# Optimization experiments

Measured on AMD Instinct MI355X. Metric: run time of the kernel, lower is better.

Reference implementation:

```python
import jax, jax.numpy as jnp
import numpy as np

FEATURE_DIM = 256
KEEP = 64  # low-frequency block size kept after the pseudo-DCT


def setup_inputs() -> dict:
    key = jax.random.key(0)
    k_x, k_w, k_b = jax.random.split(key, 3)
    B, C, H, W = 32, 3, 512, 512
    x = jax.random.uniform(k_x, (B, C, H, W), dtype=jnp.float32)
    # nn.Linear(64*64, feature_dim): weight [out, in], bias [out]
    fan_in = KEEP * KEEP
    bound = 1.0 / np.sqrt(fan_in)
    fc_w = jax.random.uniform(k_w, (FEATURE_DIM, fan_in), dtype=jnp.float32, minval=-bound, maxval=bound)
    fc_b = jax.random.uniform(k_b, (FEATURE_DIM,), dtype=jnp.float32, minval=-bound, maxval=bound)
    return {"x": x, "fc_w": fc_w, "fc_b": fc_b}


def reference(x, fc_w, fc_b):
    # grayscale conversion (input has 3 channels)
    x_gray = 0.299 * x[:, 0] + 0.587 * x[:, 1] + 0.114 * x[:, 2]  # [B, H, W]
    # "dct2d": FFT along last dim, then FFT along second-to-last, real part
    X = jnp.fft.fft(jnp.fft.fft(x_gray, axis=-1), axis=-2).real  # [B, H, W]
    # keep low-frequency 64x64 block and flatten
    coeffs = X[:, :KEEP, :KEEP].reshape(x.shape[0], KEEP * KEEP)  # [B, 4096]
    # final linear projection
    return coeffs @ fc_w.T + fc_b  # [B, feature_dim]
```

## Files before the change

kernel.cpp:

```cpp
#include <hip/hip_runtime.h>

#define HW_ (512 * 512)
#define TWOPI_512 0.01227184630308513f

typedef __attribute__((ext_vector_type(8))) _Float16 half8;
typedef __attribute__((ext_vector_type(4))) _Float16 half4;
typedef __attribute__((ext_vector_type(4))) float    f32x4;

template<bool SIN>
__device__ __forceinline__ void k1_loop(const _Float16 (*g)[520],
                                        int l15, int quad, int mk0, int mk1,
                                        f32x4& acc0, f32x4& acc1)
{
    for (int k0 = 0; k0 < 512; k0 += 32) {
        int kc = k0 + quad * 8;
        half8 bv = *(const half8*)&g[l15][kc];
        half8 a0, a1;
#pragma unroll
        for (int j = 0; j < 8; ++j) {
            int k = kc + j;
            float ang0 = (float)(__mul24(mk0, k) & 511) * TWOPI_512;
            float ang1 = (float)(__mul24(mk1, k) & 511) * TWOPI_512;
            a0[j] = (_Float16)(SIN ? __sinf(ang0) : __cosf(ang0));
            a1[j] = (_Float16)(SIN ? __sinf(ang1) : __cosf(ang1));
        }
        acc0 = __builtin_amdgcn_mfma_f32_16x16x32_f16(a0, bv, acc0, 0, 0, 0);
        acc1 = __builtin_amdgcn_mfma_f32_16x16x32_f16(a1, bv, acc1, 0, 0, 0);
    }
}

__global__ __launch_bounds__(256) void k1(const float* __restrict__ x,
                                          const float* __restrict__ fc_w,
                                          _Float16* __restrict__ PF,
                                          _Float16* __restrict__ whF)
{
    __shared__ _Float16 g[16][520];
    int t = threadIdx.x;

    if (blockIdx.x == 32) {
        int pid = blockIdx.y;
        for (int it = 0; it < 16; ++it) {
            int idx8 = pid * 4096 + it * 256 + t;
            int lane = idx8 & 63;
            int f = ((idx8 >> 6) & 15) * 16 + (lane & 15);
            int k = (idx8 >> 10) * 32 + ((lane >> 4) << 3);
            const float* wp = fc_w + (size_t)f * 4096 + k;
            float4 f0 = *(const float4*)wp;
            float4 f1 = *(const float4*)(wp + 4);
            half8 o;
            o[0] = (_Float16)(f0.x * 16.0f);
            o[1] = (_Float16)(f0.y * 16.0f);
            o[2] = (_Float16)(f0.z * 16.0f);
            o[3] = (_Float16)(f0.w * 16.0f);
            o[4] = (_Float16)(f1.x * 16.0f);
            o[5] = (_Float16)(f1.y * 16.0f);
            o[6] = (_Float16)(f1.z * 16.0f);
            o[7] = (_Float16)(f1.w * 16.0f);
            *(half8*)(whF + (size_t)idx8 * 8) = o;
        }
        return;
    }

    int h0 = blockIdx.x * 16;
    int b  = blockIdx.y;
    const float* xb = x + (size_t)b * 3 * HW_;

    for (int i = 0; i < 8; ++i) {
        int slot = t + i * 256;
        int hh = slot >> 7, w4 = slot & 127;
        const float* p = xb + (size_t)(h0 + hh) * 512 + w4 * 4;
        float4 r  = *(const float4*)p;
        float4 gg = *(const float4*)(p + HW_);
        float4 bb = *(const float4*)(p + 2 * HW_);
        half4 o;
        o.x = (_Float16)(0.299f * r.x + 0.587f * gg.x + 0.114f * bb.x);
        o.y = (_Float16)(0.299f * r.y + 0.587f * gg.y + 0.114f * bb.y);
        o.z = (_Float16)(0.299f * r.z + 0.587f * gg.z + 0.114f * bb.z);
        o.w = (_Float16)(0.299f * r.w + 0.587f * gg.w + 0.114f * bb.w);
        *(half4*)&g[hh][w4 * 4] = o;
    }
    __syncthreads();

    int lane = t & 63, wv = t >> 6, l15 = lane & 15, quad = lane >> 4;
    int mk0 = (wv * 32 + l15) & 63;
    int mk1 = (wv * 32 + 16 + l15) & 63;

    f32x4 acc[2];
    acc[0] = (f32x4){0.f, 0.f, 0.f, 0.f};
    acc[1] = (f32x4){0.f, 0.f, 0.f, 0.f};

    if (wv >= 2) k1_loop<true >(g, l15, quad, mk0, mk1, acc[0], acc[1]);
    else         k1_loop<false>(g, l15, quad, mk0, mk1, acc[0], acc[1]);

    _Float16* Pb = PF + (size_t)b * 65536;
    int h = h0 + l15;
    for (int mi = 0; mi < 2; ++mi)
        for (int r = 0; r < 4; ++r) {
            int m = wv * 32 + mi * 16 + quad * 4 + r;
            float v = acc[mi][r];
            int m64 = m & 63;
            int tt  = (m < 64) ? (h >> 5) : 16 + (h >> 5);
            if (m >= 64) v = -v;
            int lp = (m64 & 15) | (((h >> 3) & 3) << 4);
            Pb[(size_t)((tt * 4 + (m64 >> 4)) * 64 + lp) * 8 + (h & 7)] = (_Float16)v;
        }
}

template<bool SIN>
__device__ __forceinline__ void k2_loop(const _Float16* __restrict__ Pb,
                                        int t0, int kh, int quad, int lane,
                                        f32x4* acc)
{
    for (int it = 0; it < 8; ++it) {
        int tt = t0 + it;
        int kgb = tt * 32 + quad * 8;
        half8 a;
#pragma unroll
        for (int j = 0; j < 8; ++j) {
            int h = (kgb + j) & 511;
            float ang = (float)(__mul24(kh, h) & 511) * TWOPI_512;
            a[j] = (_Float16)(SIN ? __sinf(ang) : __cosf(ang));
        }
        for (int ni = 0; ni < 4; ++ni) {
            half8 bv = *(const half8*)(Pb + (size_t)((tt * 4 + ni) * 64 + lane) * 8);
            acc[ni] = __builtin_amdgcn_mfma_f32_16x16x32_f16(a, bv, acc[ni], 0, 0, 0);
        }
    }
}

__global__ __launch_bounds__(256) void k2(const _Float16* __restrict__ PF,
                                          _Float16* __restrict__ XF)
{
    __shared__ float red[3][64][17];
    int b  = blockIdx.y;
    int bx = blockIdx.x;
    int lane = threadIdx.x & 63, wv = threadIdx.x >> 6;
    int l15 = lane & 15, quad = lane >> 4;
    int kh = bx * 16 + l15;

    const _Float16* Pb = PF + (size_t)b * 65536;
    f32x4 acc[4];
    for (int i = 0; i < 4; ++i) acc[i] = (f32x4){0.f, 0.f, 0.f, 0.f};

    if (wv >= 2) k2_loop<true >(Pb, wv * 8, kh, quad, lane, acc);
    else         k2_loop<false>(Pb, wv * 8, kh, quad, lane, acc);

    if (wv)
        for (int ni = 0; ni < 4; ++ni)
            for (int r = 0; r < 4; ++r)
                red[wv - 1][lane][ni * 4 + r] = acc[ni][r];
    __syncthreads();
    if (!wv)
        for (int ni = 0; ni < 4; ++ni)
            for (int r = 0; r < 4; ++r) {
                float v = acc[ni][r] + red[0][lane][ni * 4 + r]
                                     + red[1][lane][ni * 4 + r]
                                     + red[2][lane][ni * 4 + r];
                int khr = bx * 16 + quad * 4 + r;
                int kw  = ni * 16 + l15;
                int k   = khr * 64 + kw;
                int lp  = (b & 15) | (((k >> 3) & 3) << 4);
                XF[(size_t)(((k >> 5) * 2 + (b >> 4)) * 64 + lp) * 8 + (k & 7)] =
                    (_Float16)(v * 0.0625f);
            }
}

__global__ __launch_bounds__(512) void k3(const _Float16* __restrict__ XF,
                                          const _Float16* __restrict__ whF,
                                          const float* __restrict__ fc_b,
                                          float* __restrict__ out)
{
    __shared__ float red[8][64][9];
    int nb = blockIdx.x;
    int tid = threadIdx.x;
    int lane = tid & 63, wv = tid >> 6;

    f32x4 acc[2];
    acc[0] = (f32x4){0.f, 0.f, 0.f, 0.f};
    acc[1] = (f32x4){0.f, 0.f, 0.f, 0.f};

    for (int it = 0; it < 16; ++it) {
        int tt = wv * 16 + it;
        half8 a0 = *(const half8*)(XF + (size_t)((tt * 2 + 0) * 64 + lane) * 8);
        half8 a1 = *(const half8*)(XF + (size_t)((tt * 2 + 1) * 64 + lane) * 8);
        half8 bv = *(const half8*)(whF + (size_t)((tt * 16 + nb) * 64 + lane) * 8);
        acc[0] = __builtin_amdgcn_mfma_f32_16x16x32_f16(a0, bv, acc[0], 0, 0, 0);
        acc[1] = __builtin_amdgcn_mfma_f32_16x16x32_f16(a1, bv, acc[1], 0, 0, 0);
    }

    for (int j = 0; j < 8; ++j)
        red[wv][lane][j] = acc[j >> 2][j & 3];
    __syncthreads();

    int lp = tid >> 3, j = tid & 7;
    float s = 0.f;
    for (int w = 0; w < 8; ++w) s += red[w][lp][j];
    int batch = (j >> 2) * 16 + (lp >> 4) * 4 + (j & 3);
    int f = nb * 16 + (lp & 15);
    out[batch * 256 + f] = s + fc_b[f];
}

extern "C" void kernel_launch(void* const* d_in, const int* in_sizes, int n_in,
                              void* d_out, int out_size, void* d_ws, size_t ws_size,
                              hipStream_t stream) {
    const float* x    = (const float*)d_in[0];
    const float* fc_w = (const float*)d_in[1];
    const float* fc_b = (const float*)d_in[2];
    float* out = (float*)d_out;

    char* ws = (char*)d_ws;
    _Float16* PF  = (_Float16*)(ws);
    _Float16* XF  = (_Float16*)(ws + 4194304);
    _Float16* whF = (_Float16*)(ws + 4456448);

    k1<<<dim3(33, 32), 256, 0, stream>>>(x, fc_w, PF, whF);
    k2<<<dim3(4, 32),  256, 0, stream>>>(PF, XF);
    k3<<<16, 512, 0, stream>>>(XF, whF, fc_b, out);
}
```

Measured before the change: 171.2 us.

## Use angle-addition twiddles in k1 and split-K the final projection

```diff
diff --git a/kernel.cpp b/kernel.cpp
--- a/kernel.cpp
+++ b/kernel.cpp
@@ -12,20 +12,33 @@
                                         int l15, int quad, int mk0, int mk1,
                                         f32x4& acc0, f32x4& acc1)
 {
+    float c0r[8], s0r[8], c1r[8], s1r[8];
+#pragma unroll
+    for (int j = 0; j < 8; ++j) {
+        float a0 = (float)((mk0 * j) & 511) * TWOPI_512;
+        float a1 = (float)((mk1 * j) & 511) * TWOPI_512;
+        c0r[j] = __cosf(a0); s0r[j] = __sinf(a0);
+        c1r[j] = __cosf(a1); s1r[j] = __sinf(a1);
+    }
     for (int k0 = 0; k0 < 512; k0 += 32) {
         int kc = k0 + quad * 8;
         half8 bv = *(const half8*)&g[l15][kc];
-        half8 a0, a1;
+        float b0 = (float)((mk0 * kc) & 511) * TWOPI_512;
+        float b1 = (float)((mk1 * kc) & 511) * TWOPI_512;
+        float cb0 = __cosf(b0), sb0 = __sinf(b0);
+        float cb1 = __cosf(b1), sb1 = __sinf(b1);
+        half8 a0v, a1v;
 #pragma unroll
         for (int j = 0; j < 8; ++j) {
-            int k = kc + j;
-            float ang0 = (float)(__mul24(mk0, k) & 511) * TWOPI_512;
-            float ang1 = (float)(__mul24(mk1, k) & 511) * TWOPI_512;
-            a0[j] = (_Float16)(SIN ? __sinf(ang0) : __cosf(ang0));
-            a1[j] = (_Float16)(SIN ? __sinf(ang1) : __cosf(ang1));
-        }
-        acc0 = __builtin_amdgcn_mfma_f32_16x16x32_f16(a0, bv, acc0, 0, 0, 0);
-        acc1 = __builtin_amdgcn_mfma_f32_16x16x32_f16(a1, bv, acc1, 0, 0, 0);
+            float v0 = SIN ? (sb0 * c0r[j] + cb0 * s0r[j])
+                           : (cb0 * c0r[j] - sb0 * s0r[j]);
+            float v1 = SIN ? (sb1 * c1r[j] + cb1 * s1r[j])
+                           : (cb1 * c1r[j] - sb1 * s1r[j]);
+            a0v[j] = (_Float16)v0;
+            a1v[j] = (_Float16)v1;
+        }
+        acc0 = __builtin_amdgcn_mfma_f32_16x16x32_f16(a0v, bv, acc0, 0, 0, 0);
+        acc1 = __builtin_amdgcn_mfma_f32_16x16x32_f16(a1v, bv, acc1, 0, 0, 0);
     }
 }
 
@@ -167,11 +180,11 @@
 
 __global__ __launch_bounds__(512) void k3(const _Float16* __restrict__ XF,
                                           const _Float16* __restrict__ whF,
-                                          const float* __restrict__ fc_b,
-                                          float* __restrict__ out)
+                                          float* __restrict__ wsP)
 {
     __shared__ float red[8][64][9];
-    int nb = blockIdx.x;
+    int nb = blockIdx.x & 15;
+    int kc = blockIdx.x >> 4;
     int tid = threadIdx.x;
     int lane = tid & 63, wv = tid >> 6;
 
@@ -179,8 +192,8 @@
     acc[0] = (f32x4){0.f, 0.f, 0.f, 0.f};
     acc[1] = (f32x4){0.f, 0.f, 0.f, 0.f};
 
-    for (int it = 0; it < 16; ++it) {
-        int tt = wv * 16 + it;
+    for (int it = 0; it < 2; ++it) {
+        int tt = kc * 16 + wv * 2 + it;
         half8 a0 = *(const half8*)(XF + (size_t)((tt * 2 + 0) * 64 + lane) * 8);
         half8 a1 = *(const half8*)(XF + (size_t)((tt * 2 + 1) * 64 + lane) * 8);
         half8 bv = *(const half8*)(whF + (size_t)((tt * 16 + nb) * 64 + lane) * 8);
@@ -196,8 +209,21 @@
     float s = 0.f;
     for (int w = 0; w < 8; ++w) s += red[w][lp][j];
     int batch = (j >> 2) * 16 + (lp >> 4) * 4 + (j & 3);
-    int f = nb * 16 + (lp & 15);
-    out[batch * 256 + f] = s + fc_b[f];
+    int fi = lp & 15;
+    wsP[(size_t)blockIdx.x * 512 + batch * 16 + fi] = s;
+}
+
+__global__ __launch_bounds__(256) void k4(const float* __restrict__ wsP,
+                                          const float* __restrict__ fc_b,
+                                          float* __restrict__ out)
+{
+    int gid = blockIdx.x * 256 + threadIdx.x;
+    int m = gid >> 8, f = gid & 255;
+    int nb = f >> 4, fi = f & 15;
+    float s = fc_b[f];
+    for (int kc = 0; kc < 8; ++kc)
+        s += wsP[(size_t)(kc * 16 + nb) * 512 + m * 16 + fi];
+    out[gid] = s;
 }
 
 extern "C" void kernel_launch(void* const* d_in, const int* in_sizes, int n_in,
@@ -212,8 +238,10 @@
     _Float16* PF  = (_Float16*)(ws);
     _Float16* XF  = (_Float16*)(ws + 4194304);
     _Float16* whF = (_Float16*)(ws + 4456448);
+    float*    wsP = (float*)   (ws + 6553600);
 
     k1<<<dim3(33, 32), 256, 0, stream>>>(x, fc_w, PF, whF);
     k2<<<dim3(4, 32),  256, 0, stream>>>(PF, XF);
-    k3<<<16, 512, 0, stream>>>(XF, whF, fc_b, out);
-}
+    k3<<<128, 512, 0, stream>>>(XF, whF, wsP);
+    k4<<<32, 256, 0, stream>>>(wsP, fc_b, out);
+}
```

New measurement: 162.6 us. -5.1%, faster.
